# Optimization experiments

Measured on AMD Instinct MI355X. Metric: run time of the kernel, lower is better.

The kernel has to match this reference:

```python
import jax, jax.numpy as jnp
import numpy as np

HEADS, DIM_HEADS = 16, 16
SCALE = DIM_HEADS ** -0.5

# (forward_perm, inverse_perm) for each axial dim of x: (B, S, E, H, W)
# axial axes are 1 (seq), 3 (H=4), 4 (W=5); emb axis 2 moved to last, axial axis to second-last
_PERMS = [
    ((0, 3, 4, 1, 2), (0, 3, 4, 1, 2)),  # seq axis (self-inverse)
    ((0, 1, 4, 3, 2), (0, 1, 4, 3, 2)),  # H axis (self-inverse)
    ((0, 1, 3, 4, 2), (0, 1, 4, 2, 3)),  # W axis
]


def _self_attn(x, wq, wkv, wo_w, wo_b):
    # x: (..., t, d); standard multi-head self-attention along t
    q = x @ wq.T                               # (..., t, 256)
    k, v = jnp.split(x @ wkv.T, 2, axis=-1)    # each (..., t, 256)
    lead, tlen = x.shape[:-2], x.shape[-2]
    sh = (*lead, tlen, HEADS, DIM_HEADS)
    q, k, v = q.reshape(sh), k.reshape(sh), v.reshape(sh)
    scores = jnp.einsum('...thd,...shd->...hts', q, k) * SCALE
    attn = jax.nn.softmax(scores, axis=-1)
    o = jnp.einsum('...hts,...shd->...thd', attn, v)
    o = o.reshape(*lead, tlen, HEADS * DIM_HEADS)
    return o @ wo_w.T + wo_b


def _axial_attention_layer(x, wq_l, wkv_l, wo_w_l, wo_b_l):
    # sum of attention along each axial dim (sum_axial_out=True)
    out = jnp.zeros_like(x)
    for a, (p, ip) in enumerate(_PERMS):
        y = jnp.transpose(x, p)
        y = _self_attn(y, wq_l[a], wkv_l[a], wo_w_l[a], wo_b_l[a])
        out = out + jnp.transpose(y, ip)
    return out


def setup_inputs() -> dict:
    key = jax.random.key(0)
    ks = jax.random.split(key, 8)
    B, S, E, H, W = 32, 64, 256, 4, 5
    return {
        'x': jax.random.normal(ks[0], (B, S, E, H, W), jnp.float32),
        'pos_s': jax.random.normal(ks[1], (1, S, E, 1, 1), jnp.float32),
        'pos_h': jax.random.normal(ks[2], (1, 1, E, H, 1), jnp.float32),
        'pos_w': jax.random.normal(ks[3], (1, 1, E, 1, W), jnp.float32),
        'wq': jax.random.normal(ks[4], (2, 3, 256, E), jnp.float32) * 0.02,
        'wkv': jax.random.normal(ks[5], (2, 3, 512, E), jnp.float32) * 0.02,
        'wo_w': jax.random.normal(ks[6], (2, 3, E, 256), jnp.float32) * 0.02,
        'wo_b': jnp.zeros((2, 3, E), jnp.float32),
        'dec_w': jax.random.normal(ks[7], (1, E), jnp.float32) * 0.02,
        'dec_b': jnp.zeros((1,), jnp.float32),
    }


def reference(x, pos_s, pos_h, pos_w, wq, wkv, wo_w, wo_b, dec_w, dec_b):
    # additive axial positional embeddings
    x = x + pos_s + pos_h + pos_w
    # two stacked AxialAttention blocks (no residual in the wrapper)
    for l in range(2):
        x = _axial_attention_layer(x, wq[l], wkv[l], wo_w[l], wo_b[l])
    # (B, S, E, H, W) -> (B, S, H, W, E), linear decode to 1 channel, sigmoid
    x = jnp.transpose(x, (0, 1, 3, 4, 2))
    return jax.nn.sigmoid(x @ dec_w.T + dec_b)
```

## Files before the change

kernel.cpp:

```cpp
#include <hip/hip_runtime.h>
#include <stdint.h>

typedef unsigned short u16;
typedef u16 u16x8 __attribute__((ext_vector_type(8)));
typedef __bf16 bf16x8 __attribute__((ext_vector_type(8)));
typedef float f32x4 __attribute__((ext_vector_type(4)));
typedef float f32x16 __attribute__((ext_vector_type(16)));

#define NE   256
#define NPOS 40960
#define QLD  2304

__device__ __forceinline__ float bf2f(u16 h) {
  union { unsigned u; float f; } c; c.u = ((unsigned)h) << 16; return c.f;
}
__device__ __forceinline__ u16 f2bf(float f) {
  union { float f; unsigned u; } c; c.f = f;
  unsigned u = c.u;
  return (u16)((u + 0x7FFFu + ((u >> 16) & 1u)) >> 16);
}
__device__ __forceinline__ unsigned pkbf(float a, float b) {
  unsigned r;
  asm("v_cvt_pk_bf16_f32 %0, %1, %2" : "=v"(r) : "v"(a), "v"(b));
  return r;
}
__device__ __forceinline__ void gll16(const void* g, void* l) {
  __builtin_amdgcn_global_load_lds(
      (const __attribute__((address_space(1))) void*)g,
      (__attribute__((address_space(3))) void*)l, 16, 0, 0);
}
template<int N> __device__ __forceinline__ void waitvm() {
  if constexpr (N == 0)       asm volatile("s_waitcnt vmcnt(0)"  ::: "memory");
  else if constexpr (N == 2)  asm volatile("s_waitcnt vmcnt(2)"  ::: "memory");
  else if constexpr (N == 4)  asm volatile("s_waitcnt vmcnt(4)"  ::: "memory");
  else if constexpr (N == 8)  asm volatile("s_waitcnt vmcnt(8)"  ::: "memory");
}

#define PK_T1 (6*768*256)
#define PK_T2 (2*256*768)
#define PREP_BLK 2048
#define PACK_BLK ((PK_T1 + PK_T2 + 512) / 256)
__global__ __launch_bounds__(256) void prep_pack(
    const float* __restrict__ x, const float* __restrict__ pos_s,
    const float* __restrict__ pos_h, const float* __restrict__ pos_w,
    u16* __restrict__ xb,
    const float* __restrict__ wq, const float* __restrict__ wkv,
    const float* __restrict__ wo, const float* __restrict__ wo_b,
    u16* __restrict__ wqp, u16* __restrict__ wop, float* __restrict__ bsum)
{
  __shared__ float Ls[256 * 21];
  const int tid = threadIdx.x;
  if (blockIdx.x < PREP_BLK) {
    const int bs = blockIdx.x;
    const int s  = bs & 63;
    const float* xp = x + (size_t)bs * 5120;
    for (int i = tid; i < 5120; i += 256) {
      int e = i / 20, hw = i % 20;
      int h = hw / 5, w = hw % 5;
      float v = xp[i] + pos_s[s * 256 + e] + pos_h[e * 4 + h] + pos_w[e * 5 + w];
      Ls[e * 21 + hw] = v;
    }
    __syncthreads();
    u16* op = xb + (size_t)bs * 20 * 256;
    for (int i = tid; i < 5120; i += 256) {
      int nl = i >> 8, e = i & 255;
      op[nl * 256 + e] = f2bf(Ls[e * 21 + nl]);
    }
  } else {
    int i = (blockIdx.x - PREP_BLK) * 256 + tid;
    if (i < PK_T1) {
      int la = i / (768 * 256);
      int rem = i - la * (768 * 256);
      int r = rem >> 8, c = rem & 255;
      float v = (r < 256) ? wq[(size_t)la * 65536 + r * 256 + c] * 0.25f
                          : wkv[(size_t)la * 131072 + (r - 256) * 256 + c];
      wqp[i] = f2bf(v);
    } else if (i < PK_T1 + PK_T2) {
      int j = i - PK_T1;
      int l = j / 196608;
      int rem = j - l * 196608;
      int out = rem / 768, k = rem % 768;
      int a = k >> 8, in = k & 255;
      wop[j] = f2bf(wo[(size_t)(((l * 3 + a) * 256) + out) * 256 + in]);
    } else if (i < PK_T1 + PK_T2 + 512) {
      int j = i - PK_T1 - PK_T2;
      int l = j >> 8, c = j & 255;
      bsum[j] = wo_b[(l * 3 + 0) * 256 + c] + wo_b[(l * 3 + 1) * 256 + c]
              + wo_b[(l * 3 + 2) * 256 + c];
    }
  }
}

template<int NKT, int NBN, int TPB>
__global__ __launch_bounds__(256, 2) void gemm_stream(
    const u16* __restrict__ A, const u16* __restrict__ B,
    u16* __restrict__ Cb, int ldc)
{
  constexpr int K     = NKT * 32;
  constexpr int NSTEP = NKT * TPB;
  __shared__ alignas(16) u16 As[2][128 * 32];

  const int nblk = gridDim.x;
  const int bid  = blockIdx.x;
  const int mapped = (bid & 7) * (nblk >> 3) + (bid >> 3);
  const int strip = mapped / NBN, bn = mapped % NBN;
  const int bm0 = strip * TPB;

  const int tid  = threadIdx.x;
  const int lane = tid & 63, w = tid >> 6;
  const int wr   = (w >> 1) * 64, wc = (w & 1) * 64;
  const int r16  = lane & 15, khi = lane >> 4;
  const int pofs = (khi ^ ((r16 >> 1) & 3)) * 8;

  const u16* gB = B + (size_t)bn * 128 * K;
  bf16x8 breg[NKT][4];
  #pragma unroll
  for (int kt = 0; kt < NKT; ++kt)
    #pragma unroll
    for (int n = 0; n < 4; ++n)
      breg[kt][n] = *(const bf16x8*)(gB + (size_t)(wc + n * 16 + r16) * K
                                     + kt * 32 + khi * 8);

  const u16* gA = A + (size_t)bm0 * 128 * K;
  auto STAGE_A = [&](int g) {
    const int t = g / NKT, kt = g % NKT;
    const u16* tA = gA + (size_t)t * 128 * K + kt * 32;
    u16* dst = As[g & 1];
    #pragma unroll
    for (int r = 0; r < 2; ++r) {
      int i = tid + r * 256;
      int row = i >> 2, s = i & 3;
      int ss = s ^ ((row >> 1) & 3);
      gll16(tA + (size_t)row * K + ss * 8, (char*)dst + i * 16);
    }
  };

  f32x4 acc[4][4] = {};
  STAGE_A(0);

  for (int t = 0; t < TPB; ++t) {
    #pragma unroll
    for (int kt = 0; kt < NKT; ++kt) {
      const int g = t * NKT + kt;
      if (g + 1 < NSTEP) { STAGE_A(g + 1); waitvm<2>(); }
      else               { waitvm<0>(); }
      __builtin_amdgcn_s_barrier();
      asm volatile("" ::: "memory");

      const u16* Ab = As[g & 1];
      bf16x8 af[4];
      #pragma unroll
      for (int m = 0; m < 4; ++m)
        af[m] = *(const bf16x8*)(Ab + (wr + m * 16 + r16) * 32 + pofs);
      #pragma unroll
      for (int m = 0; m < 4; ++m)
        #pragma unroll
        for (int n = 0; n < 4; ++n)
          acc[m][n] = __builtin_amdgcn_mfma_f32_16x16x32_bf16(
              af[m], breg[kt][n], acc[m][n], 0, 0, 0);

      asm volatile("" ::: "memory");
      __builtin_amdgcn_s_barrier();
    }
    const int row0 = (bm0 + t) * 128 + wr + khi * 4;
    const int col0 = bn * 128 + wc + r16;
    #pragma unroll
    for (int m = 0; m < 4; ++m)
      #pragma unroll
      for (int n = 0; n < 4; ++n)
        #pragma unroll
        for (int j = 0; j < 4; ++j) {
          Cb[(size_t)(row0 + m * 16 + j) * ldc + col0 + n * 16] = f2bf(acc[m][n][j]);
          acc[m][n][j] = 0.f;
        }
  }
}

template<int MODE, int NKT, int NBN>
__global__ __launch_bounds__(256, 2) void gemm_bt(
    const u16* __restrict__ A, const u16* __restrict__ B,
    u16* __restrict__ Cb, const float* __restrict__ bias,
    const float* __restrict__ dw, float* __restrict__ logit,
    int ldc)
{
  constexpr int K   = NKT * 32;
  constexpr int TSZ = 256 * 32;
  __shared__ alignas(16) u16 smem[3 * TSZ];

  const int bid = blockIdx.x;
  const int cpx = gridDim.x >> 3;
  const int mapped = (bid & 7) * cpx + (bid >> 3);
  const int bm = mapped / NBN, bn = mapped % NBN;

  const int tid  = threadIdx.x;
  const int lane = tid & 63, w = tid >> 6;
  const int wr   = (w >> 1) * 64, wc = (w & 1) * 64;
  const int r16  = lane & 15, khi = lane >> 4;
  const int pofs = (khi ^ ((r16 >> 1) & 3)) * 8;

  f32x4 acc[4][4] = {};

  const u16* gA = A + (size_t)bm * 128 * QLD;
  const u16* gB = B + (size_t)bn * 128 * K;

  auto STAGE = [&](int kt, int which) {
    u16* As = smem + which * TSZ;
    u16* Bsl = As + 128 * 32;
    #pragma unroll
    for (int r = 0; r < 2; ++r) {
      int i = tid + r * 256;
      int row = i >> 2, s = i & 3;
      int col = kt * 32 + (s ^ ((row >> 1) & 3)) * 8;
      int phys = (col >> 8) * 768 + (col & 255);
      gll16(gA + (size_t)row * QLD + phys, (char*)As + i * 16);
    }
    #pragma unroll
    for (int r = 0; r < 2; ++r) {
      int i = tid + r * 256;
      int row = i >> 2, s = i & 3;
      int ss = s ^ ((row >> 1) & 3);
      gll16(gB + (size_t)row * K + kt * 32 + ss * 8, (char*)Bsl + i * 16);
    }
  };

  STAGE(0, 0);
  STAGE(1, 1);
  #pragma unroll
  for (int kt = 0; kt < NKT; ++kt) {
    const int cur = kt % 3;
    if (kt + 2 < NKT)      { STAGE(kt + 2, (kt + 2) % 3); waitvm<8>(); }
    else if (kt + 1 < NKT) { waitvm<4>(); }
    else                   { waitvm<0>(); }
    __builtin_amdgcn_s_barrier();
    asm volatile("" ::: "memory");

    const u16* As = smem + cur * TSZ;
    const u16* Bsl = As + 128 * 32;
    bf16x8 af[4], bfr[4];
    #pragma unroll
    for (int m = 0; m < 4; ++m)
      af[m] = *(const bf16x8*)(As + (wr + m * 16 + r16) * 32 + pofs);
    #pragma unroll
    for (int n = 0; n < 4; ++n)
      bfr[n] = *(const bf16x8*)(Bsl + (wc + n * 16 + r16) * 32 + pofs);
    __builtin_amdgcn_s_setprio(1);
    #pragma unroll
    for (int m = 0; m < 4; ++m)
      #pragma unroll
      for (int n = 0; n < 4; ++n)
        acc[m][n] = __builtin_amdgcn_mfma_f32_16x16x32_bf16(af[m], bfr[n], acc[m][n], 0, 0, 0);
    __builtin_amdgcn_s_setprio(0);

    asm volatile("" ::: "memory");
    __builtin_amdgcn_s_barrier();
  }

  const int row0 = bm * 128 + wr + khi * 4;
  const int col0 = bn * 128 + wc + r16;

  if constexpr (MODE == 4) {
    float dwv[4], bvv[4];
    #pragma unroll
    for (int n = 0; n < 4; ++n) {
      int c = col0 + n * 16;
      dwv[n] = dw[c];
      bvv[n] = bias[c];
    }
    #pragma unroll
    for (int m = 0; m < 4; ++m) {
      #pragma unroll
      for (int j = 0; j < 4; ++j) {
        float p = 0.f;
        #pragma unroll
        for (int n = 0; n < 4; ++n) p += (acc[m][n][j] + bvv[n]) * dwv[n];
        p += __shfl_xor(p, 1);
        p += __shfl_xor(p, 2);
        p += __shfl_xor(p, 4);
        p += __shfl_xor(p, 8);
        if (r16 == 0) atomicAdd(&logit[row0 + m * 16 + j], p);
      }
    }
  } else {
    #pragma unroll
    for (int m = 0; m < 4; ++m) {
      #pragma unroll
      for (int n = 0; n < 4; ++n) {
        int c = col0 + n * 16;
        float bv = bias[c];
        #pragma unroll
        for (int j = 0; j < 4; ++j) {
          int r = row0 + m * 16 + j;
          Cb[(size_t)r * ldc + c] = f2bf(acc[m][n][j] + bv);
        }
      }
    }
  }
}

template<int T>
__device__ __forceinline__ void attn1(
    u16* __restrict__ Qb, int n, int base, int stp, int hd)
{
  u16* qp = Qb + (size_t)n * QLD + hd * 16;
  u16x8 q0 = *(const u16x8*)(qp), q1 = *(const u16x8*)(qp + 8);
  float q[16];
  #pragma unroll
  for (int d = 0; d < 8; ++d) { q[d] = bf2f(q0[d]); q[d + 8] = bf2f(q1[d]); }

  float s[T];
  float m = -1e30f;
  #pragma unroll
  for (int j = 0; j < T; ++j) {
    const u16* kp = Qb + (size_t)(base + j * stp) * QLD + 256 + hd * 16;
    u16x8 k0 = *(const u16x8*)(kp), k1 = *(const u16x8*)(kp + 8);
    float a = 0.f;
    #pragma unroll
    for (int d = 0; d < 8; ++d) a += q[d] * bf2f(k0[d]) + q[d + 8] * bf2f(k1[d]);
    s[j] = a;
    m = fmaxf(m, a);
  }
  float sum = 0.f;
  float o[16];
  #pragma unroll
  for (int d = 0; d < 16; ++d) o[d] = 0.f;
  #pragma unroll
  for (int j = 0; j < T; ++j) {
    float pj = __expf(s[j] - m);
    sum += pj;
    const u16* vp = Qb + (size_t)(base + j * stp) * QLD + 512 + hd * 16;
    u16x8 w0 = *(const u16x8*)(vp), w1 = *(const u16x8*)(vp + 8);
    #pragma unroll
    for (int d = 0; d < 8; ++d) { o[d] += pj * bf2f(w0[d]); o[d + 8] += pj * bf2f(w1[d]); }
  }
  float inv = 1.0f / sum;
  u16x8 r0, r1;
  #pragma unroll
  for (int d = 0; d < 8; ++d) { r0[d] = f2bf(o[d] * inv); r1[d] = f2bf(o[d + 8] * inv); }
  *(u16x8*)(qp)     = r0;
  *(u16x8*)(qp + 8) = r1;
}

__global__ __launch_bounds__(256) void attn_all(u16* __restrict__ QKV)
{
  if (blockIdx.x < 2560) {
    const int w = threadIdx.x >> 6, lane = threadIdx.x & 63;
    const int wid = blockIdx.x * 4 + w;
    const int hd = wid & 15, g = wid >> 4;
    const int gb = g / 20, gr = g % 20;
    const int nbase = gb * 1280 + gr;
    const int lo = lane & 31, hi = lane >> 5;

    bf16x8 kf[2], qf[2];
    #pragma unroll
    for (int t = 0; t < 2; ++t) {
      size_t r = (size_t)(nbase + (lo + 32 * t) * 20) * QLD;
      kf[t] = *(const bf16x8*)(QKV + r + 256 + hd * 16 + hi * 8);
      qf[t] = *(const bf16x8*)(QKV + r +       hd * 16 + hi * 8);
    }
    union { u16 a[8]; bf16x8 v; } vt[4];
    #pragma unroll
    for (int c = 0; c < 4; ++c)
      #pragma unroll
      for (int j = 0; j < 8; ++j)
        vt[c].a[j] = QKV[(size_t)(nbase + (c * 16 + hi * 8 + j) * 20) * QLD
                         + 512 + hd * 16 + lo];

    f32x16 s00 = {}, s10 = {}, s01 = {}, s11 = {};
    s00 = __builtin_amdgcn_mfma_f32_32x32x16_bf16(kf[0], qf[0], s00, 0, 0, 0);
    s10 = __builtin_amdgcn_mfma_f32_32x32x16_bf16(kf[1], qf[0], s10, 0, 0, 0);
    s01 = __builtin_amdgcn_mfma_f32_32x32x16_bf16(kf[0], qf[1], s01, 0, 0, 0);
    s11 = __builtin_amdgcn_mfma_f32_32x32x16_bf16(kf[1], qf[1], s11, 0, 0, 0);

    auto run_qt = [&](f32x16 t0, f32x16 t1, int qt) {
      float m = -1e30f;
      #pragma unroll
      for (int r = 0; r < 16; ++r) { m = fmaxf(m, t0[r]); m = fmaxf(m, t1[r]); }
      m = fmaxf(m, __shfl_xor(m, 32));
      const float C = 1.4426950408889634f;
      float mc = m * C;
      float sum = 0.f;
      #pragma unroll
      for (int r = 0; r < 16; ++r) {
        float p0 = __builtin_amdgcn_exp2f(t0[r] * C - mc);
        float p1 = __builtin_amdgcn_exp2f(t1[r] * C - mc);
        t0[r] = p0; t1[r] = p1; sum += p0; sum += p1;
      }
      sum += __shfl_xor(sum, 32);
      float inv = __builtin_amdgcn_rcpf(sum);
      #pragma unroll
      for (int r = 0; r < 16; ++r) { t0[r] *= inv; t1[r] *= inv; }

      f32x16 oa = {};
      #pragma unroll
      for (int c = 0; c < 4; ++c) {
        const int rb = 8 * (c & 1);
        const f32x16& tt = (c < 2) ? t0 : t1;
        unsigned X0 = pkbf(tt[rb + 0], tt[rb + 1]);
        unsigned X1 = pkbf(tt[rb + 2], tt[rb + 3]);
        unsigned Y0 = pkbf(tt[rb + 4], tt[rb + 5]);
        unsigned Y1 = pkbf(tt[rb + 6], tt[rb + 7]);
        unsigned X0p = __shfl_xor((int)X0, 32), X1p = __shfl_xor((int)X1, 32);
        unsigned Y0p = __shfl_xor((int)Y0, 32), Y1p = __shfl_xor((int)Y1, 32);
        union { unsigned u[4]; bf16x8 v; } pf;
        pf.u[0] = hi ? Y0p : X0;
        pf.u[1] = hi ? Y1p : X1;
        pf.u[2] = hi ? Y0  : X0p;
        pf.u[3] = hi ? Y1  : X1p;
        oa = __builtin_amdgcn_mfma_f32_32x32x16_bf16(vt[c].v, pf.v, oa, 0, 0, 0);
      }
      unsigned P0 = pkbf(oa[0], oa[1]);
      unsigned P1 = pkbf(oa[2], oa[3]);
      unsigned P2 = pkbf(oa[4], oa[5]);
      unsigned P3 = pkbf(oa[6], oa[7]);
      unsigned sP0 = __shfl_xor((int)P0, 32), sP1 = __shfl_xor((int)P1, 32);
      unsigned sP2 = __shfl_xor((int)P2, 32), sP3 = __shfl_xor((int)P3, 32);
      union { unsigned u[4]; u16x8 v; } ov;
      ov.u[0] = hi ? sP2 : P0;
      ov.u[1] = hi ? sP3 : P1;
      ov.u[2] = hi ? P2  : sP0;
      ov.u[3] = hi ? P3  : sP1;
      u16* po = QKV + (size_t)(nbase + (qt * 32 + lo) * 20) * QLD + hd * 16 + hi * 8;
      *(u16x8*)po = ov.v;
    };
    run_qt(s00, s10, 0);
    run_qt(s01, s11, 1);
  } else {
    const int tg = (blockIdx.x - 2560) * 256 + threadIdx.x;
    const int hd = tg & 15, n = tg >> 4;
    int h  = (n % 20) / 5;
    int w5 = n % 5;
    attn1<4>(QKV + 768,  n, n - h * 5, 5, hd);
    attn1<5>(QKV + 1536, n, n - w5,    1, hd);
  }
}

__global__ __launch_bounds__(256) void sigmoid_kernel(
    const float* __restrict__ logit, const float* __restrict__ dec_b,
    float* __restrict__ out)
{
  int i = blockIdx.x * 256 + threadIdx.x;
  out[i] = 1.0f / (1.0f + __expf(-(logit[i] + dec_b[0])));
}

extern "C" void kernel_launch(void* const* d_in, const int* in_sizes, int n_in,
                              void* d_out, int out_size, void* d_ws, size_t ws_size,
                              hipStream_t stream) {
  const float* x     = (const float*)d_in[0];
  const float* pos_s = (const float*)d_in[1];
  const float* pos_h = (const float*)d_in[2];
  const float* pos_w = (const float*)d_in[3];
  const float* wq    = (const float*)d_in[4];
  const float* wkv   = (const float*)d_in[5];
  const float* wo_w  = (const float*)d_in[6];
  const float* wo_b  = (const float*)d_in[7];
  const float* dec_w = (const float*)d_in[8];
  const float* dec_b = (const float*)d_in[9];
  float* out = (float*)d_out;

  char* ws = (char*)d_ws;
  u16*   xb    = (u16*)ws;
  u16*   QKV   = (u16*)(ws + 20971520);
  u16*   wqp   = (u16*)(ws + 209715200);
  u16*   wop   = (u16*)(ws + 212074496);
  float* bsum  = (float*)(ws + 212860928);
  float* logit = (float*)(ws + 212862976);

  prep_pack<<<PREP_BLK + PACK_BLK, 256, 0, stream>>>(
      x, pos_s, pos_h, pos_w, xb, wq, wkv, wo_w, wo_b, wqp, wop, bsum);
  hipMemsetAsync(logit, 0, NPOS * sizeof(float), stream);

  for (int l = 0; l < 2; ++l) {
    gemm_stream<8, 18, 4><<<1440, 256, 0, stream>>>(
        xb, wqp + (size_t)(l * 3) * 196608, QKV, QLD);
    attn_all<<<5120, 256, 0, stream>>>(QKV);
    if (l == 0)
      gemm_bt<3, 24, 2><<<640, 256, 0, stream>>>(
          QKV, wop, xb, bsum, nullptr, nullptr, 256);
    else
      gemm_bt<4, 24, 2><<<640, 256, 0, stream>>>(
          QKV, wop + 196608, nullptr, bsum + 256, dec_w, logit, 0);
  }

  sigmoid_kernel<<<NPOS / 256, 256, 0, stream>>>(logit, dec_b, out);
}
```

Measured before the change: 326.4 us.

## Replace streaming B-in-register QKV GEMM with 256x256 tiled triple-buffered GEMM

The QKV projection GEMM changes from 128x128 tiles that hold B in registers and stream four A tiles per block to 512-thread blocks computing 256x256 output tiles. Both A and B are staged into LDS with a three-buffer global_load_lds pipeline, and s_setprio is raised around the MFMA loop. The aim is more reuse per LDS load and better latency hiding. In exchange it uses more LDS (96KB per block) and more accumulator registers, which may lower occupancy, and the grid is 1440 blocks of 256x256 covering 40960x2304.

```diff
diff --git a/kernel.cpp b/kernel.cpp
--- a/kernel.cpp
+++ b/kernel.cpp
@@ -33,6 +33,7 @@
   if constexpr (N == 0)       asm volatile("s_waitcnt vmcnt(0)"  ::: "memory");
   else if constexpr (N == 2)  asm volatile("s_waitcnt vmcnt(2)"  ::: "memory");
   else if constexpr (N == 4)  asm volatile("s_waitcnt vmcnt(4)"  ::: "memory");
+  else if constexpr (N == 6)  asm volatile("s_waitcnt vmcnt(6)"  ::: "memory");
   else if constexpr (N == 8)  asm volatile("s_waitcnt vmcnt(8)"  ::: "memory");
 }
 
@@ -91,89 +92,94 @@
   }
 }
 
-template<int NKT, int NBN, int TPB>
-__global__ __launch_bounds__(256, 2) void gemm_stream(
+template<int NKT, int NBN>
+__global__ __launch_bounds__(512, 2) void gemm256(
     const u16* __restrict__ A, const u16* __restrict__ B,
     u16* __restrict__ Cb, int ldc)
 {
-  constexpr int K     = NKT * 32;
-  constexpr int NSTEP = NKT * TPB;
-  __shared__ alignas(16) u16 As[2][128 * 32];
-
-  const int nblk = gridDim.x;
-  const int bid  = blockIdx.x;
-  const int mapped = (bid & 7) * (nblk >> 3) + (bid >> 3);
-  const int strip = mapped / NBN, bn = mapped % NBN;
-  const int bm0 = strip * TPB;
+  constexpr int K   = NKT * 32;
+  constexpr int TSZ = 512 * 32;
+  __shared__ alignas(16) u16 smem[3 * TSZ];
+
+  const int bid = blockIdx.x;
+  const int cpx = gridDim.x >> 3;
+  const int mapped = (bid & 7) * cpx + (bid >> 3);
+  const int bm = mapped / NBN, bn = mapped % NBN;
 
   const int tid  = threadIdx.x;
   const int lane = tid & 63, w = tid >> 6;
-  const int wr   = (w >> 1) * 64, wc = (w & 1) * 64;
+  const int wr   = (w >> 2) * 128;
+  const int wc   = (w & 3) * 64;
   const int r16  = lane & 15, khi = lane >> 4;
   const int pofs = (khi ^ ((r16 >> 1) & 3)) * 8;
 
-  const u16* gB = B + (size_t)bn * 128 * K;
-  bf16x8 breg[NKT][4];
-  #pragma unroll
-  for (int kt = 0; kt < NKT; ++kt)
+  f32x4 acc[8][4] = {};
+
+  const u16* gA = A + (size_t)bm * 256 * K;
+  const u16* gB = B + (size_t)bn * 256 * K;
+
+  auto STAGE = [&](int kt, int which) {
+    u16* As = smem + which * TSZ;
+    u16* Bs = As + 256 * 32;
+    const u16* tA = gA + kt * 32;
+    const u16* tB = gB + kt * 32;
+    #pragma unroll
+    for (int r = 0; r < 2; ++r) {
+      int i = tid + r * 512;
+      int row = i >> 2, c = i & 3;
+      int cs = c ^ ((row >> 1) & 3);
+      gll16(tA + (size_t)row * K + cs * 8, (char*)As + i * 16);
+    }
+    #pragma unroll
+    for (int r = 0; r < 2; ++r) {
+      int i = tid + r * 512;
+      int row = i >> 2, c = i & 3;
+      int cs = c ^ ((row >> 1) & 3);
+      gll16(tB + (size_t)row * K + cs * 8, (char*)Bs + i * 16);
+    }
+  };
+
+  STAGE(0, 0);
+  STAGE(1, 1);
+  #pragma unroll
+  for (int kt = 0; kt < NKT; ++kt) {
+    const int cur = kt % 3;
+    if (kt + 2 < NKT)      { STAGE(kt + 2, (kt + 2) % 3); waitvm<8>(); }
+    else if (kt + 1 < NKT) { waitvm<4>(); }
+    else                   { waitvm<0>(); }
+    __builtin_amdgcn_s_barrier();
+    asm volatile("" ::: "memory");
+
+    const u16* As = smem + cur * TSZ;
+    const u16* Bs = As + 256 * 32;
+    bf16x8 af[8], bfr[4];
+    #pragma unroll
+    for (int m = 0; m < 8; ++m)
+      af[m] = *(const bf16x8*)(As + (wr + m * 16 + r16) * 32 + pofs);
     #pragma unroll
     for (int n = 0; n < 4; ++n)
-      breg[kt][n] = *(const bf16x8*)(gB + (size_t)(wc + n * 16 + r16) * K
-                                     + kt * 32 + khi * 8);
-
-  const u16* gA = A + (size_t)bm0 * 128 * K;
-  auto STAGE_A = [&](int g) {
-    const int t = g / NKT, kt = g % NKT;
-    const u16* tA = gA + (size_t)t * 128 * K + kt * 32;
-    u16* dst = As[g & 1];
-    #pragma unroll
-    for (int r = 0; r < 2; ++r) {
-      int i = tid + r * 256;
-      int row = i >> 2, s = i & 3;
-      int ss = s ^ ((row >> 1) & 3);
-      gll16(tA + (size_t)row * K + ss * 8, (char*)dst + i * 16);
-    }
-  };
-
-  f32x4 acc[4][4] = {};
-  STAGE_A(0);
-
-  for (int t = 0; t < TPB; ++t) {
-    #pragma unroll
-    for (int kt = 0; kt < NKT; ++kt) {
-      const int g = t * NKT + kt;
-      if (g + 1 < NSTEP) { STAGE_A(g + 1); waitvm<2>(); }
-      else               { waitvm<0>(); }
-      __builtin_amdgcn_s_barrier();
-      asm volatile("" ::: "memory");
-
-      const u16* Ab = As[g & 1];
-      bf16x8 af[4];
-      #pragma unroll
-      for (int m = 0; m < 4; ++m)
-        af[m] = *(const bf16x8*)(Ab + (wr + m * 16 + r16) * 32 + pofs);
-      #pragma unroll
-      for (int m = 0; m < 4; ++m)
-        #pragma unroll
-        for (int n = 0; n < 4; ++n)
-          acc[m][n] = __builtin_amdgcn_mfma_f32_16x16x32_bf16(
-              af[m], breg[kt][n], acc[m][n], 0, 0, 0);
-
-      asm volatile("" ::: "memory");
-      __builtin_amdgcn_s_barrier();
-    }
-    const int row0 = (bm0 + t) * 128 + wr + khi * 4;
-    const int col0 = bn * 128 + wc + r16;
-    #pragma unroll
-    for (int m = 0; m < 4; ++m)
+      bfr[n] = *(const bf16x8*)(Bs + (wc + n * 16 + r16) * 32 + pofs);
+    __builtin_amdgcn_s_setprio(1);
+    #pragma unroll
+    for (int m = 0; m < 8; ++m)
       #pragma unroll
       for (int n = 0; n < 4; ++n)
-        #pragma unroll
-        for (int j = 0; j < 4; ++j) {
-          Cb[(size_t)(row0 + m * 16 + j) * ldc + col0 + n * 16] = f2bf(acc[m][n][j]);
-          acc[m][n][j] = 0.f;
-        }
-  }
+        acc[m][n] = __builtin_amdgcn_mfma_f32_16x16x32_bf16(af[m], bfr[n], acc[m][n], 0, 0, 0);
+    __builtin_amdgcn_s_setprio(0);
+
+    asm volatile("" ::: "memory");
+    __builtin_amdgcn_s_barrier();
+  }
+
+  const int row0 = bm * 256 + wr + khi * 4;
+  const int col0 = bn * 256 + wc + r16;
+  #pragma unroll
+  for (int m = 0; m < 8; ++m)
+    #pragma unroll
+    for (int n = 0; n < 4; ++n)
+      #pragma unroll
+      for (int j = 0; j < 4; ++j)
+        Cb[(size_t)(row0 + m * 16 + j) * ldc + col0 + n * 16] = f2bf(acc[m][n][j]);
 }
 
 template<int MODE, int NKT, int NBN>
@@ -470,7 +476,7 @@
   hipMemsetAsync(logit, 0, NPOS * sizeof(float), stream);
 
   for (int l = 0; l < 2; ++l) {
-    gemm_stream<8, 18, 4><<<1440, 256, 0, stream>>>(
+    gemm256<8, 9><<<1440, 512, 0, stream>>>(
         xb, wqp + (size_t)(l * 3) * 196608, QKV, QLD);
     attn_all<<<5120, 256, 0, stream>>>(QKV);
     if (l == 0)
```

Result: no change. 328.1 us (+0.5%).
